# Optimization experiments

Measured on AMD Instinct MI355X. Metric: run time of the kernel, lower is better.

## Reference

```python
import jax, jax.numpy as jnp
import numpy as np

# dims: B=1, T=2048 (prefill), dim=3072, Hq=32, Hkv=8, D=128, S=max_seq_len=4096

def _rotate_interleave(x):
    # (-x1, x0, -x3, x2, ...) pairwise rotation on last dim
    x = x.reshape(x.shape[:-1] + (-1, 2))
    x = jnp.stack((-x[..., 1], x[..., 0]), axis=-1)
    return x.reshape(x.shape[:-2] + (-1,))


def setup_inputs() -> dict:
    key = jax.random.key(0)
    ks = jax.random.split(key, 8)
    B, T, DIM, HQ, HKV, HD, S = 1, 2048, 3072, 32, 8, 128, 4096
    x = jax.random.normal(ks[0], (B, T, DIM), jnp.float32)
    wq = jax.random.normal(ks[1], (HQ * HD, DIM), jnp.float32) * 0.02
    wk = jax.random.normal(ks[2], (HKV * HD, DIM), jnp.float32) * 0.02
    wv = jax.random.normal(ks[3], (HKV * HD, DIM), jnp.float32) * 0.02
    wo = jax.random.normal(ks[4], (DIM, HQ * HD), jnp.float32) * 0.02
    freqs_cos = jax.random.uniform(ks[5], (T, HD), jnp.float32)
    freqs_sin = jax.random.uniform(ks[6], (T, HD), jnp.float32)
    input_pos = jnp.zeros((1,), jnp.int32)
    k_cache = jnp.zeros((1, S, HKV, HD), jnp.float32)
    v_cache = jnp.zeros((1, S, HKV, HD), jnp.float32)
    return {"x": x, "wq": wq, "wk": wk, "wv": wv, "wo": wo,
            "freqs_cos": freqs_cos, "freqs_sin": freqs_sin,
            "k_cache": k_cache, "v_cache": v_cache, "input_pos": input_pos}


def reference(x, wq, wk, wv, wo, freqs_cos, freqs_sin, k_cache, v_cache, input_pos):
    B, T, _ = x.shape
    HQ, HKV, HD = 32, 8, 128
    q = (x @ wq.T).reshape(B, T, HQ, HD)
    k = (x @ wk.T).reshape(B, T, HKV, HD)
    v = (x @ wv.T).reshape(B, T, HKV, HD)
    # interleaved RoPE (computed in fp32 as in apply_rotary_emb)
    fc = freqs_cos[None, :, None, :]
    fs = freqs_sin[None, :, None, :]
    q = q * fc + _rotate_interleave(q) * fs
    k = k * fc + _rotate_interleave(k) * fs
    # KV-cache update at start_pos (torch.ops.llama.update_cache)
    sp = input_pos[0]
    k_all = jax.lax.dynamic_update_slice(k_cache, k, (0, sp, 0, 0))  # [1,S,HKV,HD]
    v_all = jax.lax.dynamic_update_slice(v_cache, v, (0, sp, 0, 0))
    S = k_all.shape[1]
    # GQA: expand kv heads to match q heads (head h -> kv head h // rep)
    rep = HQ // HKV
    kr = jnp.repeat(k_all, rep, axis=2)  # [1,S,HQ,HD]
    vr = jnp.repeat(v_all, rep, axis=2)
    scale = 1.0 / np.sqrt(HD).astype(np.float32)
    scores = jnp.einsum('bthd,bshd->bhts', q, kr) * scale  # [B,HQ,T,S]
    # causal mask relative to start_pos (custom_sdpa is_causal=True path)
    qpos = sp + jnp.arange(T)
    kpos = jnp.arange(S)
    mask = kpos[None, :] <= qpos[:, None]                   # [T,S]
    scores = jnp.where(mask[None, None], scores, jnp.float32(-1e30))
    attn = jax.nn.softmax(scores, axis=-1)
    y = jnp.einsum('bhts,bshd->bthd', attn, vr).reshape(B, T, HQ * HD)
    return y @ wo.T
```

## Files before the change

### kernel.cpp

```cpp
#include <hip/hip_runtime.h>
#include <hip/hip_bf16.h>
#include <stdint.h>

typedef float f32x4 __attribute__((ext_vector_type(4)));
typedef short s16x8 __attribute__((ext_vector_type(8)));
typedef short s16x4 __attribute__((ext_vector_type(4)));
typedef unsigned short u16x2 __attribute__((ext_vector_type(2)));
typedef unsigned short u16x4 __attribute__((ext_vector_type(4)));

#define AS1 __attribute__((address_space(1)))
#define AS3 __attribute__((address_space(3)))

static constexpr int T_    = 2048;
static constexpr int DIM_  = 3072;
static constexpr int HQ_   = 32;
static constexpr int HKV_  = 8;
static constexpr int HD_   = 128;
static constexpr int S_    = 4096;
static constexpr int NQKV_ = HQ_ * HD_ + 2 * HKV_ * HD_;

__device__ __forceinline__ unsigned short f2b(float f) {
  return __builtin_bit_cast(unsigned short, __float2bfloat16(f));
}
__device__ __forceinline__ float b2f(unsigned short u) {
  return __bfloat162float(__builtin_bit_cast(__hip_bfloat16, u));
}
__device__ __forceinline__ float exp2a(float x) {
  float r; asm("v_exp_f32 %0, %1" : "=v"(r) : "v"(x)); return r;
}

__device__ __forceinline__ void gld_lds16(const void* g, void* l) {
  __builtin_amdgcn_global_load_lds((AS1 unsigned int*)(uintptr_t)g,
                                   (AS3 unsigned int*)l, 16, 0, 0);
}

#define FENCE() asm volatile("" ::: "memory")
#define BAR()   do { FENCE(); __builtin_amdgcn_s_barrier(); FENCE(); } while (0)
#define WAIT_VM(n)   asm volatile("s_waitcnt vmcnt(" #n ")" ::: "memory")
#define WAIT_LGKM(n) asm volatile("s_waitcnt lgkmcnt(" #n ")" ::: "memory")
#define SCHEDB()     __builtin_amdgcn_sched_barrier(0)

__global__ __launch_bounds__(256)
void k_cvt(const float* __restrict__ src, unsigned short* __restrict__ dst, int n4) {
  int i = blockIdx.x * 256 + threadIdx.x;
  if (i >= n4) return;
  float4 v = reinterpret_cast<const float4*>(src)[i];
  u16x4 o;
  o.x = f2b(v.x); o.y = f2b(v.y); o.z = f2b(v.z); o.w = f2b(v.w);
  reinterpret_cast<u16x4*>(dst)[i] = o;
}

template<bool OUT_BF16>
__global__ __launch_bounds__(512, 2)
void k_gemm256(const unsigned short* __restrict__ A,
               const unsigned short* __restrict__ B,
               void* __restrict__ Cout, int N, int K, int KT,
               int nbn, int xcdq, int k0step, int partStride) {
  __shared__ unsigned short lds_u[2][32768];
  char* ldsBase = (char*)&lds_u[0][0];

  const int bid = blockIdx.x;
  const int swz = (bid & 7) * xcdq + (bid >> 3);
  const int bm  = swz / nbn, bn = swz % nbn;
  const int tid = threadIdx.x, lane = tid & 63, wid = tid >> 6;
  const int wm  = wid >> 2, wn = wid & 3;
  const int r16 = lane & 15, q4 = lane >> 4;
  const int k0  = blockIdx.y * k0step;

  const unsigned short* Ag = A + (size_t)(bm * 256) * K + k0;
  const unsigned short* Bg = B + (size_t)(bn * 256) * K + k0;

  const int srow = tid >> 3;
  const int scol = ((tid & 7) ^ (srow & 7)) * 8;

  f32x4 acc[8][4] = {};
  s16x8 afA[4][2], afB[4][2], bfA[2][2], bfB[2][2];

  auto stageA = [&](int c, int r, int t) {
    gld_lds16(Ag + (size_t)(r * 64 + srow) * K + t * 64 + scol,
              ldsBase + c * 65536 + r * 8192 + tid * 16);
  };
  auto stageB = [&](int c, int r, int t) {
    gld_lds16(Bg + (size_t)(r * 64 + srow) * K + t * 64 + scol,
              ldsBase + c * 65536 + 32768 + r * 8192 + tid * 16);
  };
  auto stagePair = [&](int c, int pair, int t) {
    switch (pair) {
      case 0: stageB(c, 0, t); stageB(c, 1, t); break;
      case 1: stageB(c, 2, t); stageB(c, 3, t); break;
      case 2: stageA(c, 0, t); stageA(c, 2, t); break;
      case 3: stageA(c, 1, t); stageA(c, 3, t); break;
    }
  };
  auto readAF = [&](s16x8 (&dst)[4][2], char* base, int rowoff) {
    #pragma unroll
    for (int i = 0; i < 4; ++i) {
      const int arow = wm * 128 + rowoff + i * 16 + r16;
      #pragma unroll
      for (int kk = 0; kk < 2; ++kk)
        dst[i][kk] = *(const s16x8*)(base + arow * 128 +
                                     (((kk * 4 + q4) ^ (arow & 7)) << 4));
    }
  };
  auto readBF = [&](s16x8 (&dst)[2][2], char* base, int rowoff) {
    #pragma unroll
    for (int j = 0; j < 2; ++j) {
      const int brow = wn * 64 + rowoff + j * 16 + r16;
      #pragma unroll
      for (int kk = 0; kk < 2; ++kk)
        dst[j][kk] = *(const s16x8*)(base + 32768 + brow * 128 +
                                     (((kk * 4 + q4) ^ (brow & 7)) << 4));
    }
  };

#define MFMA16(AF, BF, IO, JO)                                                 \
  __builtin_amdgcn_s_setprio(1);                                               \
  _Pragma("unroll")                                                            \
  for (int i_ = 0; i_ < 4; ++i_) {                                             \
    _Pragma("unroll")                                                          \
    for (int j_ = 0; j_ < 2; ++j_) {                                           \
      _Pragma("unroll")                                                        \
      for (int kk_ = 0; kk_ < 2; ++kk_)                                        \
        acc[(IO) + i_][(JO) + j_] = __builtin_amdgcn_mfma_f32_16x16x32_bf16(   \
            AF[i_][kk_], BF[j_][kk_], acc[(IO) + i_][(JO) + j_], 0, 0, 0);     \
    }                                                                          \
  }                                                                            \
  __builtin_amdgcn_s_setprio(0);

  stagePair(0, 0, 0); stagePair(0, 1, 0); stagePair(0, 2, 0); stagePair(0, 3, 0);
  stagePair(1, 0, 1); stagePair(1, 1, 1);
  WAIT_VM(6);
  BAR();
  readAF(afA, ldsBase, 0);
  readBF(bfA, ldsBase, 0);

  for (int t = 0; t < KT - 2; ++t) {
    const int c = t & 1;
    char* baseC = ldsBase + c * 65536;
    char* baseN = ldsBase + (c ^ 1) * 65536;
    readBF(bfB, baseC, 32);
    stagePair(c ^ 1, 2, t + 1);
    WAIT_VM(6); BAR();
    WAIT_LGKM(4); SCHEDB();
    MFMA16(afA, bfA, 0, 0);
    BAR();
    readAF(afB, baseC, 64);
    stagePair(c ^ 1, 3, t + 1);
    BAR();
    WAIT_LGKM(8); SCHEDB();
    MFMA16(afA, bfB, 0, 2);
    BAR();
    stagePair(c, 0, t + 2);
    WAIT_VM(4); BAR();
    WAIT_LGKM(0); SCHEDB();
    MFMA16(afB, bfA, 4, 0);
    BAR();
    readAF(afA, baseN, 0);
    readBF(bfA, baseN, 0);
    stagePair(c, 1, t + 2);
    WAIT_VM(8); BAR();
    WAIT_LGKM(12); SCHEDB();
    MFMA16(afB, bfB, 4, 2);
    BAR();
  }

  {
    const int t = KT - 2;
    const int c = t & 1;
    char* baseC = ldsBase + c * 65536;
    char* baseN = ldsBase + (c ^ 1) * 65536;
    readBF(bfB, baseC, 32);
    stagePair(c ^ 1, 2, t + 1);
    WAIT_VM(6); BAR();
    WAIT_LGKM(4); SCHEDB();
    MFMA16(afA, bfA, 0, 0);
    BAR();
    readAF(afB, baseC, 64);
    stagePair(c ^ 1, 3, t + 1);
    BAR();
    WAIT_LGKM(8); SCHEDB();
    MFMA16(afA, bfB, 0, 2);
    BAR();
    WAIT_VM(2); BAR();
    WAIT_LGKM(0); SCHEDB();
    MFMA16(afB, bfA, 4, 0);
    BAR();
    readAF(afA, baseN, 0);
    readBF(bfA, baseN, 0);
    WAIT_VM(4); BAR();
    WAIT_LGKM(12); SCHEDB();
    MFMA16(afB, bfB, 4, 2);
    BAR();
  }
  {
    const int t = KT - 1;
    char* baseC = ldsBase + (t & 1) * 65536;
    readBF(bfB, baseC, 32);
    WAIT_VM(0); BAR();
    WAIT_LGKM(4); SCHEDB();
    MFMA16(afA, bfA, 0, 0);
    BAR();
    readAF(afB, baseC, 64);
    BAR();
    WAIT_LGKM(8); SCHEDB();
    MFMA16(afA, bfB, 0, 2);
    BAR();
    WAIT_LGKM(0); SCHEDB();
    MFMA16(afB, bfA, 4, 0);
    MFMA16(afB, bfB, 4, 2);
  }
#undef MFMA16

  #pragma unroll
  for (int fi = 0; fi < 8; ++fi) {
    const int row = bm * 256 + wm * 128 + fi * 16 + q4 * 4;
    #pragma unroll
    for (int fj = 0; fj < 4; ++fj) {
      const int col = bn * 256 + wn * 64 + fj * 16 + r16;
      if constexpr (OUT_BF16) {
        unsigned short* C = (unsigned short*)Cout;
        #pragma unroll
        for (int rr = 0; rr < 4; ++rr)
          C[(size_t)(row + rr) * N + col] = f2b(acc[fi][fj][rr]);
      } else {
        float* C = (float*)Cout + (size_t)blockIdx.y * partStride;
        #pragma unroll
        for (int rr = 0; rr < 4; ++rr)
          C[(size_t)(row + rr) * N + col] = acc[fi][fj][rr];
      }
    }
  }
}

__global__ __launch_bounds__(256)
void k_add(const f32x4* __restrict__ a, const f32x4* __restrict__ b,
           f32x4* __restrict__ o, int n4) {
  int i = blockIdx.x * 256 + threadIdx.x;
  const int stride = gridDim.x * 256;
  for (; i < n4; i += stride) o[i] = a[i] + b[i];
}

__global__ __launch_bounds__(256)
void k_rope_q(const unsigned short* __restrict__ qkv,
              const float* __restrict__ fc, const float* __restrict__ fs,
              unsigned short* __restrict__ Qr) {
  int idx = blockIdx.x * 256 + threadIdx.x;
  int t   = idx >> 11;
  int rem = idx & 2047;
  int h   = rem >> 6;
  int d0  = (rem & 63) << 1;
  size_t qoff = (size_t)t * NQKV_ + h * HD_ + d0;
  u16x2 xv = *reinterpret_cast<const u16x2*>(&qkv[qoff]);
  float x0 = b2f(xv.x), x1 = b2f(xv.y);
  float c0 = fc[t * HD_ + d0], c1 = fc[t * HD_ + d0 + 1];
  float s0 = fs[t * HD_ + d0], s1 = fs[t * HD_ + d0 + 1];
  u16x2 o;
  o.x = f2b(x0 * c0 - x1 * s0);
  o.y = f2b(x1 * c1 + x0 * s1);
  *reinterpret_cast<u16x2*>(&Qr[((size_t)h * T_ + t) * HD_ + d0]) = o;
}

__global__ __launch_bounds__(256)
void k_rope_k(const unsigned short* __restrict__ qkv,
              const float* __restrict__ fc, const float* __restrict__ fs,
              unsigned short* __restrict__ Kall, const int* __restrict__ ipos) {
  int idx = blockIdx.x * 256 + threadIdx.x;
  int t   = idx >> 9;
  int rem = idx & 511;
  int hk  = rem >> 6;
  int d0  = (rem & 63) << 1;
  int sp  = ipos[0];
  size_t qoff = (size_t)t * NQKV_ + HQ_ * HD_ + hk * HD_ + d0;
  u16x2 xv = *reinterpret_cast<const u16x2*>(&qkv[qoff]);
  float x0 = b2f(xv.x), x1 = b2f(xv.y);
  float c0 = fc[t * HD_ + d0], c1 = fc[t * HD_ + d0 + 1];
  float s0 = fs[t * HD_ + d0], s1 = fs[t * HD_ + d0 + 1];
  unsigned short o0 = f2b(x0 * c0 - x1 * s0);
  unsigned short o1 = f2b(x1 * c1 + x0 * s1);
  size_t ooff = ((size_t)hk * S_ + sp + t) * HD_ + d0;
  Kall[ooff] = o0; Kall[ooff + 1] = o1;
}

__global__ __launch_bounds__(256)
void k_prefix(const float* __restrict__ kc, const float* __restrict__ vc,
              unsigned short* __restrict__ Kall, unsigned short* __restrict__ VT,
              const int* __restrict__ ipos) {
  int sp = ipos[0];
  int total = sp * HKV_ * HD_;
  for (int idx = blockIdx.x * 256 + threadIdx.x; idx < total;
       idx += gridDim.x * 256) {
    int s   = idx >> 10;
    int rem = idx & 1023;
    int hk  = rem >> 7;
    int d   = rem & 127;
    Kall[((size_t)hk * S_ + s) * HD_ + d] = f2b(kc[((size_t)s * HKV_ + hk) * HD_ + d]);
    VT[((size_t)hk * HD_ + d) * S_ + s]   = f2b(vc[((size_t)s * HKV_ + hk) * HD_ + d]);
  }
}

__global__ __launch_bounds__(256)
void k_vt(const unsigned short* __restrict__ qkv,
          unsigned short* __restrict__ VT, const int* __restrict__ ipos) {
  int hk = blockIdx.x >> 5;
  int tt = blockIdx.x & 31;
  int sp = ipos[0];
  __shared__ unsigned short lds[64][136];
  int tid = threadIdx.x;
  #pragma unroll
  for (int p = 0; p < 4; ++p) {
    int e   = p * 256 + tid;
    int tr  = e >> 4;
    int col = (e & 15) << 3;
    *reinterpret_cast<s16x8*>(&lds[tr][col]) =
        *reinterpret_cast<const s16x8*>(&qkv[(size_t)(tt * 64 + tr) * NQKV_ + (HQ_ + HKV_) * HD_ + hk * HD_ + col]);
  }
  __syncthreads();
  #pragma unroll
  for (int p = 0; p < 32; ++p) {
    int e = p * 256 + tid;
    int d = e >> 6;
    int t = e & 63;
    VT[((size_t)hk * HD_ + d) * S_ + sp + tt * 64 + t] = lds[t][d];
  }
}

__global__ __launch_bounds__(256, 4)
void k_attn(const unsigned short* __restrict__ Qr,
            const unsigned short* __restrict__ Kall,
            const unsigned short* __restrict__ VT,
            unsigned short* __restrict__ Y,
            const int* __restrict__ ipos) {
  constexpr int QB = 64, KB = 64;
  const int bid  = blockIdx.x;
  const int hk   = bid & 7;
  const int j2   = bid >> 3;
  const int h    = hk * 4 + (j2 & 3);
  const int qt   = j2 >> 2;
  const int sp   = ipos[0];
  const int tid  = threadIdx.x, lane = tid & 63, wave = tid >> 6;
  const int r16  = lane & 15, q4 = lane >> 4;
  const float NEG_INF = -__builtin_inff();
  const float MINIT   = -1.0e30f;

  __shared__ unsigned short Ks[KB][HD_ + 8];
  __shared__ unsigned short Vs[HD_][KB + 8];

  const int qbase = qt * QB + wave * 16;
  s16x8 qf[4];
  const unsigned short* qp = Qr + ((size_t)h * T_ + qbase + r16) * HD_;
  #pragma unroll
  for (int ki = 0; ki < 4; ++ki)
    qf[ki] = *reinterpret_cast<const s16x8*>(qp + ki * 32 + q4 * 8);

  f32x4 o[8] = {};
  float m = MINIT, l = 0.f;
  const int qpos = sp + qbase + r16;
  const int qpos_wave_max = sp + qbase + 15;
  int jmax = (sp + qt * QB + QB - 1) >> 6;
  if (jmax > S_ / KB - 1) jmax = S_ / KB - 1;
  const float scale2 = 0.12751744416312068f;

  const unsigned short* Kbase = Kall + (size_t)hk * S_ * HD_;
  const unsigned short* Vbase = VT + (size_t)hk * HD_ * S_;

  for (int j = 0; j <= jmax; ++j) {
    s16x8 kreg[4], vreg[4];
    #pragma unroll
    for (int p = 0; p < 4; ++p) {
      int e  = p * 256 + tid;
      int kr = e >> 4, kc = (e & 15) << 3;
      kreg[p] = *reinterpret_cast<const s16x8*>(Kbase + (size_t)(j * KB + kr) * HD_ + kc);
      int vd = e >> 3, vs = (e & 7) << 3;
      vreg[p] = *reinterpret_cast<const s16x8*>(Vbase + (size_t)vd * S_ + j * KB + vs);
    }
    __syncthreads();
    #pragma unroll
    for (int p = 0; p < 4; ++p) {
      int e  = p * 256 + tid;
      int kr = e >> 4, kc = (e & 15) << 3;
      *reinterpret_cast<s16x8*>(&Ks[kr][kc]) = kreg[p];
      int vd = e >> 3, vs = (e & 7) << 3;
      *reinterpret_cast<s16x8*>(&Vs[vd][vs]) = vreg[p];
    }
    __syncthreads();

    const bool active = (j * KB <= qpos_wave_max);
    if (active) {
      f32x4 sfr[4];
      #pragma unroll
      for (int fn = 0; fn < 4; ++fn) {
        sfr[fn] = f32x4{0.f, 0.f, 0.f, 0.f};
        #pragma unroll
        for (int ki = 0; ki < 4; ++ki) {
          s16x8 kf = *reinterpret_cast<const s16x8*>(&Ks[fn * 16 + r16][ki * 32 + q4 * 8]);
          sfr[fn] = __builtin_amdgcn_mfma_f32_16x16x32_bf16(kf, qf[ki], sfr[fn], 0, 0, 0);
        }
      }
      float p[16];
      const bool needMask = (j * KB + KB - 1) > (sp + qbase);
      if (needMask) {
        const int kb = j * KB + q4 * 4;
        #pragma unroll
        for (int fn = 0; fn < 4; ++fn)
          #pragma unroll
          for (int r = 0; r < 4; ++r)
            p[fn * 4 + r] = (kb + fn * 16 + r <= qpos) ? sfr[fn][r] * scale2 : NEG_INF;
      } else {
        #pragma unroll
        for (int fn = 0; fn < 4; ++fn)
          #pragma unroll
          for (int r = 0; r < 4; ++r)
            p[fn * 4 + r] = sfr[fn][r] * scale2;
      }
      float pmax = p[0];
      #pragma unroll
      for (int i = 1; i < 16; ++i) pmax = fmaxf(pmax, p[i]);
      pmax = fmaxf(pmax, __shfl_xor(pmax, 16));
      pmax = fmaxf(pmax, __shfl_xor(pmax, 32));
      if (!__all(pmax <= m + 8.0f)) {
        float mn = fmaxf(m, pmax);
        float alpha = exp2a(m - mn);
        m = mn; l *= alpha;
        #pragma unroll
        for (int r = 0; r < 4; ++r) {
          float aq = __shfl(alpha, q4 * 4 + r);
          #pragma unroll
          for (int db = 0; db < 8; ++db) o[db][r] *= aq;
        }
      }
      float rs = 0.f;
      #pragma unroll
      for (int i = 0; i < 16; ++i) { p[i] = exp2a(p[i] - m); rs += p[i]; }
      rs += __shfl_xor(rs, 16); rs += __shfl_xor(rs, 32);
      l += rs;
      s16x8 pf[2];
      #pragma unroll
      for (int w = 0; w < 2; ++w)
        #pragma unroll
        for (int i = 0; i < 8; ++i)
          pf[w][i] = (short)f2b(p[w * 8 + i]);
      #pragma unroll
      for (int w = 0; w < 2; ++w) {
        const int cb = w * 32 + q4 * 4;
        #pragma unroll
        for (int db = 0; db < 8; ++db) {
          s16x4 va = *reinterpret_cast<const s16x4*>(&Vs[db * 16 + r16][cb]);
          s16x4 vb = *reinterpret_cast<const s16x4*>(&Vs[db * 16 + r16][cb + 16]);
          s16x8 vf = __builtin_shufflevector(va, vb, 0, 1, 2, 3, 4, 5, 6, 7);
          o[db] = __builtin_amdgcn_mfma_f32_16x16x32_bf16(pf[w], vf, o[db], 0, 0, 0);
        }
      }
    }
  }

  float rcpl = 1.0f / l;
  float rlq[4];
  #pragma unroll
  for (int r = 0; r < 4; ++r) rlq[r] = __shfl(rcpl, q4 * 4 + r);
  #pragma unroll
  for (int db = 0; db < 8; ++db)
    #pragma unroll
    for (int r = 0; r < 4; ++r) {
      int t = qt * QB + wave * 16 + q4 * 4 + r;
      int d = db * 16 + r16;
      Y[(size_t)t * (HQ_ * HD_) + h * HD_ + d] = f2b(o[db][r] * rlq[r]);
    }
}

extern "C" void kernel_launch(void* const* d_in, const int* in_sizes, int n_in,
                              void* d_out, int out_size, void* d_ws, size_t ws_size,
                              hipStream_t stream) {
  const float* x  = (const float*)d_in[0];
  const float* wq = (const float*)d_in[1];
  const float* wk = (const float*)d_in[2];
  const float* wv = (const float*)d_in[3];
  const float* wo = (const float*)d_in[4];
  const float* fc = (const float*)d_in[5];
  const float* fs = (const float*)d_in[6];
  const float* kc = (const float*)d_in[7];
  const float* vc = (const float*)d_in[8];
  const int* ipos = (const int*)d_in[9];

  char* ws = (char*)d_ws;
  unsigned short* xb   = (unsigned short*)(ws);
  unsigned short* wqkv = (unsigned short*)(ws + 12582912);
  unsigned short* qkv  = (unsigned short*)(ws + 50331648);
  unsigned short* Qr   = (unsigned short*)(ws + 75497472);
  unsigned short* Kall = (unsigned short*)(ws + 92274688);
  unsigned short* VT   = (unsigned short*)(ws + 100663296);
  unsigned short* wo_b = (unsigned short*)(ws);
  unsigned short* y    = qkv;

  float* part0 = (float*)(ws + 12582912);
  float* part1 = (float*)(ws + 75497472);
  const int partStrideElems = (75497472 - 12582912) / 4;

  k_cvt<<<6144, 256, 0, stream>>>(x, xb, 6291456 / 4);
  k_cvt<<<12288, 256, 0, stream>>>(wq, wqkv, 12582912 / 4);
  k_cvt<<<3072, 256, 0, stream>>>(wk, wqkv + 12582912, 3145728 / 4);
  k_cvt<<<3072, 256, 0, stream>>>(wv, wqkv + 15728640, 3145728 / 4);

  k_gemm256<true><<<192, 512, 0, stream>>>(xb, wqkv, qkv, NQKV_, DIM_, 48, 24, 24, 0, 0);

  k_cvt<<<12288, 256, 0, stream>>>(wo, wo_b, 12582912 / 4);

  k_rope_q<<<16384, 256, 0, stream>>>(qkv, fc, fs, Qr);
  k_rope_k<<<4096, 256, 0, stream>>>(qkv, fc, fs, Kall, ipos);
  k_prefix<<<2048, 256, 0, stream>>>(kc, vc, Kall, VT, ipos);
  k_vt<<<256, 256, 0, stream>>>(qkv, VT, ipos);

  k_attn<<<1024, 256, 0, stream>>>(Qr, Kall, VT, y, ipos);

  k_gemm256<false><<<dim3(96, 2), 512, 0, stream>>>(y, wo_b, part0, DIM_, HQ_ * HD_,
                                                    32, 12, 12, 2048, partStrideElems);
  k_add<<<1024, 256, 0, stream>>>((const f32x4*)part0, (const f32x4*)part1,
                                  (f32x4*)d_out, 6291456 / 4);
}
```

Before: 304.7 us.

## Double-buffer attention K/V tiles with direct global-to-LDS loads and XOR swizzle

The attention kernel now stages K and V tiles straight from global memory into a double-buffered LDS region, prefetching the next tile while the current one is computed. This replaces the register round-trip and the two barriers per iteration. An XOR swizzle on the LDS layout replaces the padding to avoid bank conflicts. Q tiles are also launched in reverse order so the longest causal blocks start first. Occupancy bounds drop from 4 to 2 blocks per CU to fit the 64KB LDS buffer, which may reduce latency hiding.

```diff
diff --git a/kernel.cpp b/kernel.cpp
--- a/kernel.cpp
+++ b/kernel.cpp
@@ -163,7 +163,6 @@
     MFMA16(afB, bfB, 4, 2);
     BAR();
   }
-
   {
     const int t = KT - 2;
     const int c = t & 1;
@@ -324,33 +323,55 @@
   }
 }
 
-__global__ __launch_bounds__(256, 4)
+__global__ __launch_bounds__(256, 2)
 void k_attn(const unsigned short* __restrict__ Qr,
             const unsigned short* __restrict__ Kall,
             const unsigned short* __restrict__ VT,
             unsigned short* __restrict__ Y,
             const int* __restrict__ ipos) {
   constexpr int QB = 64, KB = 64;
+  __shared__ char lds[65536];
   const int bid  = blockIdx.x;
   const int hk   = bid & 7;
   const int j2   = bid >> 3;
   const int h    = hk * 4 + (j2 & 3);
-  const int qt   = j2 >> 2;
-  const int sp   = ipos[0];
+  const int qt   = 31 - (j2 >> 2);
   const int tid  = threadIdx.x, lane = tid & 63, wave = tid >> 6;
   const int r16  = lane & 15, q4 = lane >> 4;
+  const int vx   = r16 & 7;
   const float NEG_INF = -__builtin_inff();
   const float MINIT   = -1.0e30f;
 
-  __shared__ unsigned short Ks[KB][HD_ + 8];
-  __shared__ unsigned short Vs[HD_][KB + 8];
-
+  const int sp = ipos[0];
   const int qbase = qt * QB + wave * 16;
+  const unsigned short* Kbase = Kall + (size_t)hk * S_ * HD_;
+  const unsigned short* Vbase = VT + (size_t)hk * HD_ * S_;
+
   s16x8 qf[4];
   const unsigned short* qp = Qr + ((size_t)h * T_ + qbase + r16) * HD_;
   #pragma unroll
   for (int ki = 0; ki < 4; ++ki)
     qf[ki] = *reinterpret_cast<const s16x8*>(qp + ki * 32 + q4 * 8);
+  SCHEDB(); WAIT_VM(0); SCHEDB();
+
+  auto stage = [&](int c, int jt) {
+    #pragma unroll
+    for (int p = 0; p < 4; ++p) {
+      int e  = p * 256 + tid;
+      int kr = e >> 4;
+      int ks = (e & 15) ^ (kr & 7);
+      gld_lds16(Kbase + (size_t)(jt * KB + kr) * HD_ + ks * 8,
+                lds + c * 16384 + e * 16);
+    }
+    #pragma unroll
+    for (int p = 0; p < 4; ++p) {
+      int e  = p * 256 + tid;
+      int vd = e >> 3;
+      int vs = (e & 7) ^ (vd & 7);
+      gld_lds16(Vbase + (size_t)vd * S_ + jt * KB + vs * 8,
+                lds + 32768 + c * 16384 + e * 16);
+    }
+  };
 
   f32x4 o[8] = {};
   float m = MINIT, l = 0.f;
@@ -360,51 +381,38 @@
   if (jmax > S_ / KB - 1) jmax = S_ / KB - 1;
   const float scale2 = 0.12751744416312068f;
 
-  const unsigned short* Kbase = Kall + (size_t)hk * S_ * HD_;
-  const unsigned short* Vbase = VT + (size_t)hk * HD_ * S_;
+  stage(0, 0);
 
   for (int j = 0; j <= jmax; ++j) {
-    s16x8 kreg[4], vreg[4];
-    #pragma unroll
-    for (int p = 0; p < 4; ++p) {
-      int e  = p * 256 + tid;
-      int kr = e >> 4, kc = (e & 15) << 3;
-      kreg[p] = *reinterpret_cast<const s16x8*>(Kbase + (size_t)(j * KB + kr) * HD_ + kc);
-      int vd = e >> 3, vs = (e & 7) << 3;
-      vreg[p] = *reinterpret_cast<const s16x8*>(Vbase + (size_t)vd * S_ + j * KB + vs);
-    }
-    __syncthreads();
-    #pragma unroll
-    for (int p = 0; p < 4; ++p) {
-      int e  = p * 256 + tid;
-      int kr = e >> 4, kc = (e & 15) << 3;
-      *reinterpret_cast<s16x8*>(&Ks[kr][kc]) = kreg[p];
-      int vd = e >> 3, vs = (e & 7) << 3;
-      *reinterpret_cast<s16x8*>(&Vs[vd][vs]) = vreg[p];
-    }
-    __syncthreads();
+    const int c = j & 1;
+    if (j < jmax) { stage(c ^ 1, j + 1); WAIT_VM(8); }
+    else         { WAIT_VM(0); }
+    BAR();
 
     const bool active = (j * KB <= qpos_wave_max);
     if (active) {
+      const char* kb = lds + c * 16384;
+      const char* vb = lds + 32768 + c * 16384;
       f32x4 sfr[4];
       #pragma unroll
       for (int fn = 0; fn < 4; ++fn) {
         sfr[fn] = f32x4{0.f, 0.f, 0.f, 0.f};
         #pragma unroll
         for (int ki = 0; ki < 4; ++ki) {
-          s16x8 kf = *reinterpret_cast<const s16x8*>(&Ks[fn * 16 + r16][ki * 32 + q4 * 8]);
+          s16x8 kf = *(const s16x8*)(kb + (fn * 16 + r16) * 256 +
+                                     (((ki * 4 + q4) ^ vx) << 4));
           sfr[fn] = __builtin_amdgcn_mfma_f32_16x16x32_bf16(kf, qf[ki], sfr[fn], 0, 0, 0);
         }
       }
       float p[16];
       const bool needMask = (j * KB + KB - 1) > (sp + qbase);
       if (needMask) {
-        const int kb = j * KB + q4 * 4;
+        const int kbp = j * KB + q4 * 4;
         #pragma unroll
         for (int fn = 0; fn < 4; ++fn)
           #pragma unroll
           for (int r = 0; r < 4; ++r)
-            p[fn * 4 + r] = (kb + fn * 16 + r <= qpos) ? sfr[fn][r] * scale2 : NEG_INF;
+            p[fn * 4 + r] = (kbp + fn * 16 + r <= qpos) ? sfr[fn][r] * scale2 : NEG_INF;
       } else {
         #pragma unroll
         for (int fn = 0; fn < 4; ++fn)
@@ -439,18 +447,21 @@
         #pragma unroll
         for (int i = 0; i < 8; ++i)
           pf[w][i] = (short)f2b(p[w * 8 + i]);
+      const int voff = (q4 & 1) * 8;
+      const int sbase = q4 >> 1;
       #pragma unroll
       for (int w = 0; w < 2; ++w) {
-        const int cb = w * 32 + q4 * 4;
         #pragma unroll
         for (int db = 0; db < 8; ++db) {
-          s16x4 va = *reinterpret_cast<const s16x4*>(&Vs[db * 16 + r16][cb]);
-          s16x4 vb = *reinterpret_cast<const s16x4*>(&Vs[db * 16 + r16][cb + 16]);
-          s16x8 vf = __builtin_shufflevector(va, vb, 0, 1, 2, 3, 4, 5, 6, 7);
+          const char* vr = vb + (db * 16 + r16) * 128 + voff;
+          s16x4 va = *(const s16x4*)(vr + (((w * 4 + sbase) ^ vx) << 4));
+          s16x4 vb2 = *(const s16x4*)(vr + (((w * 4 + 2 + sbase) ^ vx) << 4));
+          s16x8 vf = __builtin_shufflevector(va, vb2, 0, 1, 2, 3, 4, 5, 6, 7);
           o[db] = __builtin_amdgcn_mfma_f32_16x16x32_bf16(pf[w], vf, o[db], 0, 0, 0);
         }
       }
     }
+    BAR();
   }
 
   float rcpl = 1.0f / l;
```

After: 287.3 us. -5.7%, faster.
